# Kernel tuning notes

Measured on AMD Instinct MI355X. Metric: run time of the kernel, lower is better.

## Reference

```python
import jax, jax.numpy as jnp
import numpy as np

B, L = 512, 16

def setup_inputs() -> dict:
    key = jax.random.key(0)
    k1, k2 = jax.random.split(key)
    y_true = jax.random.randint(k1, (B, L), 0, 2, dtype=jnp.int32)
    y_pred = jax.random.normal(k2, (B, L), dtype=jnp.float32)
    return {"y_true": y_true, "y_pred": y_pred}

def reference(y_true, y_pred):
    b = y_true.shape[0]
    yt = y_true.reshape(b, -1)
    yp = y_pred.reshape(b, -1)
    l = yp.shape[1]
    mp = (yt == 1).astype(yp.dtype)          # [B,L] positive-row mask per label
    mn = 1.0 - mp                             # [B,L] negative-row mask per label
    n_pos = mp.sum(axis=0)                    # [L]
    n_neg = mn.sum(axis=0)                    # [L]
    # Torch selects FULL rows for pos/neg then flattens, so for each label the
    # hinge pairs every element of a positive row with every element of a
    # negative row. S[i,j] = sum_{c,d} relu(1 - yp[i,c] + yp[j,d]) is shared
    # across labels; only the row masks differ per label.
    T = jax.nn.relu(1.0 - yp[:, :, None, None] + yp[None, None, :, :])  # [B,L,B,L]
    S = T.sum(axis=(1, 3))                    # [B,B]
    per_label = jnp.einsum('il,ij,jl->l', mp, S, mn)  # sum over pos rows i, neg rows j
    # weight * mean = (1/(np*nn)) * sum / (np*L * nn*L) = sum / (np^2 * nn^2 * L^2)
    denom = (n_pos * n_neg) ** 2 * (l * l)
    valid = (n_pos > 0) & (n_neg > 0)
    loss = jnp.sum(jnp.where(valid, per_label / jnp.where(valid, denom, 1.0), 0.0))
    return loss
```

## Files before the change

kernel.cpp:

```cpp
#include <hip/hip_runtime.h>

#define NROWS 512
#define NLAB  16
#define TILE  16
#define GRIDX (NROWS / TILE)
#define NBLK  (GRIDX * GRIDX)

__global__ __launch_bounds__(256) void auc_pair(const int* __restrict__ yt,
                                                const float* __restrict__ yp,
                                                float* __restrict__ partial) {
    __shared__ float ya[TILE][TILE];
    __shared__ float yb[TILE][TILE];
    __shared__ float S_tile[TILE][TILE + 1];
    __shared__ unsigned posA[TILE];
    __shared__ unsigned posB[TILE];

    const int bx = blockIdx.x;
    const int i0 = (bx >> 5) * TILE;
    const int j0 = (bx & 31) * TILE;
    const int t  = threadIdx.x;
    const int r  = t >> 4;
    const int c  = t & 15;

    ya[r][c] = yp[(i0 + r) * NLAB + c];
    yb[r][c] = yp[(j0 + r) * NLAB + c] + 1.0f;
    {
        unsigned long long ba = __ballot(yt[(i0 + r) * NLAB + c] == 1);
        unsigned long long bb = __ballot(yt[(j0 + r) * NLAB + c] == 1);
        if (c == 0) {
            posA[r] = (unsigned)((ba >> ((r & 3) * 16)) & 0xFFFFull);
            posB[r] = (unsigned)((bb >> ((r & 3) * 16)) & 0xFFFFull);
        }
    }
    __syncthreads();

    float a[TILE], b[TILE];
    #pragma unroll
    for (int k = 0; k < TILE; ++k) a[k] = ya[r][k];
    #pragma unroll
    for (int k = 0; k < TILE; ++k) b[k] = yb[c][k];

    float S = 0.0f;
    #pragma unroll
    for (int d = 0; d < TILE; ++d) {
        #pragma unroll
        for (int cc = 0; cc < TILE; ++cc) {
            S += fmaxf(b[d] - a[cc], 0.0f);
        }
    }
    S_tile[r][c] = S;
    __syncthreads();

    {
        const int l = r, ti = c;
        float rowsum = 0.0f;
        #pragma unroll
        for (int tj = 0; tj < TILE; ++tj) {
            if (((~posB[tj]) >> l) & 1u) rowsum += S_tile[ti][tj];
        }
        float val = ((posA[ti] >> l) & 1u) ? rowsum : 0.0f;
        val += __shfl_xor(val, 1);
        val += __shfl_xor(val, 2);
        val += __shfl_xor(val, 4);
        val += __shfl_xor(val, 8);
        if (ti == 0) partial[bx * NLAB + l] = val;
    }
}

__global__ __launch_bounds__(256) void auc_reduce(const int* __restrict__ yt,
                                                  const float* __restrict__ partial,
                                                  float* __restrict__ out) {
    __shared__ float lsum[16][NLAB];
    __shared__ int   lcnt[16][NLAB];
    __shared__ float pl_s[NLAB];
    __shared__ int   pl_c[NLAB];

    const int t = threadIdx.x;
    const int lab = t & 15;
    const int grp = t >> 4;

    float s = 0.0f;
    #pragma unroll 16
    for (int k = 0; k < NBLK / 16; ++k) {
        s += partial[t + 256 * k];
    }
    lsum[grp][lab] = s;

    int cnt = 0;
    #pragma unroll 8
    for (int k = 0; k < NROWS / 16; ++k) {
        cnt += (yt[(grp + 16 * k) * NLAB + lab] == 1) ? 1 : 0;
    }
    lcnt[grp][lab] = cnt;
    __syncthreads();

    if (t < NLAB) {
        float ps = 0.0f;
        int pc = 0;
        #pragma unroll
        for (int g = 0; g < 16; ++g) {
            ps += lsum[g][t];
            pc += lcnt[g][t];
        }
        pl_s[t] = ps;
        pl_c[t] = pc;
    }
    __syncthreads();

    if (t == 0) {
        double loss = 0.0;
        #pragma unroll
        for (int l = 0; l < NLAB; ++l) {
            const int np_ = pl_c[l];
            const int nn_ = NROWS - np_;
            if (np_ > 0 && nn_ > 0) {
                const double prod = (double)np_ * (double)nn_;
                const double denom = prod * prod * (double)(NLAB * NLAB);
                loss += (double)pl_s[l] / denom;
            }
        }
        out[0] = (float)loss;
    }
}

extern "C" void kernel_launch(void* const* d_in, const int* in_sizes, int n_in,
                              void* d_out, int out_size, void* d_ws, size_t ws_size,
                              hipStream_t stream) {
    const int* y_true = (const int*)d_in[0];
    const float* y_pred = (const float*)d_in[1];
    float* out = (float*)d_out;
    float* partial = (float*)d_ws;

    auc_pair<<<NBLK, 256, 0, stream>>>(y_true, y_pred, partial);
    auc_reduce<<<1, 256, 0, stream>>>(y_true, partial, out);
}
```

Baseline: 64.52 us.

## Fuse pair and reduce kernels into one launch with per-block atomic accumulation

Merges the pairwise hinge kernel and the final reduction kernel into a single kernel. Each block now recounts the positives per label from all of y_true, applies the per-label normalisation itself, and atomically adds its weighted contribution to the output. This removes the second launch and the round trip of partial sums through the workspace. In exchange, every block re-reads the full label array, which adds redundant global/L2 traffic. The result also depends on the output buffer being zeroed before the launch, and float atomics make the summation order nondeterministic.

```diff
diff --git a/kernel.cpp b/kernel.cpp
--- a/kernel.cpp
+++ b/kernel.cpp
@@ -6,14 +6,16 @@
 #define GRIDX (NROWS / TILE)
 #define NBLK  (GRIDX * GRIDX)
 
-__global__ __launch_bounds__(256) void auc_pair(const int* __restrict__ yt,
-                                                const float* __restrict__ yp,
-                                                float* __restrict__ partial) {
+__global__ __launch_bounds__(256) void auc_single(const int* __restrict__ yt,
+                                                  const float* __restrict__ yp,
+                                                  float* __restrict__ out) {
     __shared__ float ya[TILE][TILE];
     __shared__ float yb[TILE][TILE];
     __shared__ float S_tile[TILE][TILE + 1];
     __shared__ unsigned posA[TILE];
     __shared__ unsigned posB[TILE];
+    __shared__ int   lcnt[16][NLAB];
+    __shared__ float wsum[NLAB];
 
     const int bx = blockIdx.x;
     const int i0 = (bx >> 5) * TILE;
@@ -32,6 +34,12 @@
             posB[r] = (unsigned)((bb >> ((r & 3) * 16)) & 0xFFFFull);
         }
     }
+
+    int cnt = 0;
+    #pragma unroll 8
+    for (int k = 0; k < NROWS / 16; ++k) {
+        cnt += (yt[(r + 16 * k) * NLAB + c] == 1) ? 1 : 0;
+    }
     __syncthreads();
 
     float a[TILE], b[TILE];
@@ -49,77 +57,40 @@
         }
     }
     S_tile[r][c] = S;
+    lcnt[r][c] = cnt;
     __syncthreads();
 
-    {
-        const int l = r, ti = c;
-        float rowsum = 0.0f;
+    const int l = r, ti = c;
+    float rowsum = 0.0f;
+    #pragma unroll
+    for (int tj = 0; tj < TILE; ++tj) {
+        if (((~posB[tj]) >> l) & 1u) rowsum += S_tile[ti][tj];
+    }
+    float val = ((posA[ti] >> l) & 1u) ? rowsum : 0.0f;
+    val += __shfl_xor(val, 1);
+    val += __shfl_xor(val, 2);
+    val += __shfl_xor(val, 4);
+    val += __shfl_xor(val, 8);
+
+    if (c == 0) {
+        int np_ = 0;
         #pragma unroll
-        for (int tj = 0; tj < TILE; ++tj) {
-            if (((~posB[tj]) >> l) & 1u) rowsum += S_tile[ti][tj];
+        for (int g = 0; g < 16; ++g) np_ += lcnt[g][r];
+        const int nn_ = NROWS - np_;
+        float w = 0.0f;
+        if (np_ > 0 && nn_ > 0) {
+            const double prod = (double)np_ * (double)nn_;
+            w = (float)((double)val / (prod * prod * (double)(NLAB * NLAB)));
         }
-        float val = ((posA[ti] >> l) & 1u) ? rowsum : 0.0f;
-        val += __shfl_xor(val, 1);
-        val += __shfl_xor(val, 2);
-        val += __shfl_xor(val, 4);
-        val += __shfl_xor(val, 8);
-        if (ti == 0) partial[bx * NLAB + l] = val;
-    }
-}
-
-__global__ __launch_bounds__(256) void auc_reduce(const int* __restrict__ yt,
-                                                  const float* __restrict__ partial,
-                                                  float* __restrict__ out) {
-    __shared__ float lsum[16][NLAB];
-    __shared__ int   lcnt[16][NLAB];
-    __shared__ float pl_s[NLAB];
-    __shared__ int   pl_c[NLAB];
-
-    const int t = threadIdx.x;
-    const int lab = t & 15;
-    const int grp = t >> 4;
-
-    float s = 0.0f;
-    #pragma unroll 16
-    for (int k = 0; k < NBLK / 16; ++k) {
-        s += partial[t + 256 * k];
-    }
-    lsum[grp][lab] = s;
-
-    int cnt = 0;
-    #pragma unroll 8
-    for (int k = 0; k < NROWS / 16; ++k) {
-        cnt += (yt[(grp + 16 * k) * NLAB + lab] == 1) ? 1 : 0;
-    }
-    lcnt[grp][lab] = cnt;
-    __syncthreads();
-
-    if (t < NLAB) {
-        float ps = 0.0f;
-        int pc = 0;
-        #pragma unroll
-        for (int g = 0; g < 16; ++g) {
-            ps += lsum[g][t];
-            pc += lcnt[g][t];
-        }
-        pl_s[t] = ps;
-        pl_c[t] = pc;
+        wsum[r] = w;
     }
     __syncthreads();
 
     if (t == 0) {
-        double loss = 0.0;
+        float s = 0.0f;
         #pragma unroll
-        for (int l = 0; l < NLAB; ++l) {
-            const int np_ = pl_c[l];
-            const int nn_ = NROWS - np_;
-            if (np_ > 0 && nn_ > 0) {
-                const double prod = (double)np_ * (double)nn_;
-                const double denom = prod * prod * (double)(NLAB * NLAB);
-                loss += (double)pl_s[l] / denom;
-            }
-        }
-        out[0] = (float)loss;
+        for (int g = 0; g < NLAB; ++g) s += wsum[g];
+        atomicAdd(out, s);
     }
 }
 
@@ -129,8 +100,6 @@
     const int* y_true = (const int*)d_in[0];
     const float* y_pred = (const float*)d_in[1];
     float* out = (float*)d_out;
-    float* partial = (float*)d_ws;
 
-    auc_pair<<<NBLK, 256, 0, stream>>>(y_true, y_pred, partial);
-    auc_reduce<<<1, 256, 0, stream>>>(y_true, partial, out);
+    auc_single<<<NBLK, 256, 0, stream>>>(y_true, y_pred, out);
 }
```

Measured after the change: 71.15 us. 1.1x slower.
